# Performance work log

Hardware: AMD Instinct MI355X
Metric: run time of the kernel (lower is better)

## Reference

```python
import jax, jax.numpy as jnp
import numpy as np

NUM_STATES = 64
HIDDEN = 32
NUM_ACTIONS = 3
SEQ_LEN = 512
BATCH = 2048


def setup_inputs() -> dict:
    key = jax.random.key(0)
    ks = jax.random.split(key, 7)
    s_ih = 1.0 / np.sqrt(HIDDEN)
    x = jax.random.normal(ks[0], (SEQ_LEN, BATCH, NUM_STATES), dtype=jnp.float32)
    # PyTorch LSTM params: gate order [i, f, g, o], each block of size HIDDEN
    W_ih = jax.random.uniform(ks[1], (4 * HIDDEN, NUM_STATES), minval=-s_ih, maxval=s_ih, dtype=jnp.float32)
    W_hh = jax.random.uniform(ks[2], (4 * HIDDEN, HIDDEN), minval=-s_ih, maxval=s_ih, dtype=jnp.float32)
    b_ih = jax.random.uniform(ks[3], (4 * HIDDEN,), minval=-s_ih, maxval=s_ih, dtype=jnp.float32)
    b_hh = jax.random.uniform(ks[4], (4 * HIDDEN,), minval=-s_ih, maxval=s_ih, dtype=jnp.float32)
    s_d = 1.0 / np.sqrt(HIDDEN)
    W_d = jax.random.uniform(ks[5], (NUM_ACTIONS, HIDDEN), minval=-s_d, maxval=s_d, dtype=jnp.float32)
    b_d = jax.random.uniform(ks[6], (NUM_ACTIONS,), minval=-s_d, maxval=s_d, dtype=jnp.float32)
    return {"x": x, "W_ih": W_ih, "W_hh": W_hh, "b_ih": b_ih, "b_hh": b_hh, "W_d": W_d, "b_d": b_d}


def _lstm_last_hidden(x, W_ih, W_hh, b_ih, b_hh):
    # x: [T, B, F] time-major, as in nn.LSTM(batch_first=False)
    B = x.shape[1]
    H = W_hh.shape[1]
    # Precompute input projections for all timesteps in one GEMM: [T, B, 4H]
    x_proj = jnp.einsum('tbf,gf->tbg', x, W_ih) + (b_ih + b_hh)

    def step(carry, xp_t):
        h, c = carry
        gates = xp_t + h @ W_hh.T  # [B, 4H]
        i, f, g, o = jnp.split(gates, 4, axis=-1)
        i = jax.nn.sigmoid(i)
        f = jax.nn.sigmoid(f)
        g = jnp.tanh(g)
        o = jax.nn.sigmoid(o)
        c = f * c + i * g
        h = o * jnp.tanh(c)
        return (h, c), None

    h0 = jnp.zeros((B, H), dtype=x.dtype)
    c0 = jnp.zeros((B, H), dtype=x.dtype)
    (h_T, _), _ = jax.lax.scan(step, (h0, c0), x_proj)
    return h_T  # [B, H] == lstm output at last timestep (x[-1,:,:])


def reference(x, W_ih, W_hh, b_ih, b_hh, W_d, b_d):
    h_T = _lstm_last_hidden(x, W_ih, W_hh, b_ih, b_hh)
    h = jax.nn.relu(h_T)
    return h @ W_d.T + b_d  # [B, num_actions]
```

## Files before the change

kernel.cpp:

```cpp
#include <hip/hip_runtime.h>

typedef __bf16 bf16_t;
typedef __bf16 bf16x8 __attribute__((ext_vector_type(8)));
typedef float  f32x4  __attribute__((ext_vector_type(4)));
typedef unsigned int u32x4 __attribute__((ext_vector_type(4)));

#define T_STEPS 512
#define BATCH   2048
#define NS      64
#define FSTR    36

#define K_SIG  (-1.4426950408889634f)
#define K_TANH ( 2.8853900817779268f)

#define MFMA(A, B, C) __builtin_amdgcn_mfma_f32_16x16x32_bf16((A), (B), (C), 0, 0, 0)
#define RCPE(xv) __builtin_amdgcn_rcpf(1.0f + __builtin_amdgcn_exp2f(xv))

__device__ __forceinline__ void barrier_lgkm() {
  asm volatile("s_waitcnt lgkmcnt(0)\n\ts_barrier" ::: "memory");
}

__global__ __launch_bounds__(256, 1) __attribute__((amdgpu_waves_per_eu(1, 1)))
void lstm_policy_kernel(const float* __restrict__ x,
                        const float* __restrict__ W_ih,
                        const float* __restrict__ W_hh,
                        const float* __restrict__ b_ih,
                        const float* __restrict__ b_hh,
                        const float* __restrict__ W_d,
                        const float* __restrict__ b_d,
                        float* __restrict__ out)
{
  __shared__ unsigned int hlds[2][4][64];
  __shared__ float hf[16 * FSTR];

  const int tid  = threadIdx.x;
  const int wv   = tid >> 6;
  const int lane = tid & 63;
  const int m    = lane & 15;
  const int q    = lane >> 4;
  const int U    = wv >> 1;
  const int rsel = wv & 1;
  const int row0 = blockIdx.x << 4;

  bf16x8 a_ih[4][2], a_hh[4];
  f32x4  bias[4];
  #pragma unroll
  for (int G = 0; G < 4; ++G) {
    const float k = (G == 2) ? K_TANH : K_SIG;
    const int wrow = (G << 5) + (U << 4) + m;
    const float* pih = W_ih + wrow * 64;
    const float* phh = W_hh + (wrow << 5);
    #pragma unroll
    for (int j = 0; j < 8; ++j) {
      a_ih[G][0][j] = (bf16_t)(k * pih[(q << 3) + j]);
      a_ih[G][1][j] = (bf16_t)(k * pih[32 + (q << 3) + j]);
      const int us = (j < 4) ? ((q << 2) + j) : (16 + (q << 2) + (j - 4));
      a_hh[G][j] = (bf16_t)(k * phh[us]);
    }
    #pragma unroll
    for (int r = 0; r < 4; ++r) {
      const int u = (G << 5) + (U << 4) + (q << 2) + r;
      bias[G][r] = (b_ih[u] + b_hh[u]) * k;
    }
  }

  const size_t xstep = (size_t)BATCH * NS;
  const float* xb = x + (size_t)row0 * NS;
  const int    lo = m * NS + (q << 3);

  f32x4 xf[4][4];
  {
    const float* p1 = xb + 1 * xstep + lo;
    const float* p2 = xb + 2 * xstep + lo;
    const float* p3 = xb + 3 * xstep + lo;
    const float* p4 = xb + 4 * xstep + lo;
    xf[1][0]=*(const f32x4*)(p1); xf[1][1]=*(const f32x4*)(p1+4); xf[1][2]=*(const f32x4*)(p1+32); xf[1][3]=*(const f32x4*)(p1+36);
    xf[2][0]=*(const f32x4*)(p2); xf[2][1]=*(const f32x4*)(p2+4); xf[2][2]=*(const f32x4*)(p2+32); xf[2][3]=*(const f32x4*)(p2+36);
    xf[3][0]=*(const f32x4*)(p3); xf[3][1]=*(const f32x4*)(p3+4); xf[3][2]=*(const f32x4*)(p3+32); xf[3][3]=*(const f32x4*)(p3+36);
    xf[0][0]=*(const f32x4*)(p4); xf[0][1]=*(const f32x4*)(p4+4); xf[0][2]=*(const f32x4*)(p4+32); xf[0][3]=*(const f32x4*)(p4+36);
  }

  f32x4 acc[4];
  {
    const float* p0 = xb + lo;
    f32x4 x0a = *(const f32x4*)(p0),      x0b = *(const f32x4*)(p0 + 4);
    f32x4 x0c = *(const f32x4*)(p0 + 32), x0d = *(const f32x4*)(p0 + 36);
    bf16x8 xA, xB;
    #pragma unroll
    for (int j = 0; j < 4; ++j) {
      xA[j] = (bf16_t)x0a[j]; xA[4+j] = (bf16_t)x0b[j];
      xB[j] = (bf16_t)x0c[j]; xB[4+j] = (bf16_t)x0d[j];
    }
    #pragma unroll
    for (int G = 0; G < 4; ++G) {
      acc[G] = MFMA(a_ih[G][0], xA, bias[G]);
      acc[G] = MFMA(a_ih[G][1], xB, acc[G]);
    }
  }

  float cst[2] = {0.0f, 0.0f};
  bf16x8 hB = {};

  #define CELL(RR, E, HOUT)                                                         \
    {                                                                               \
      const float iv = RCPE(gr[0][RR]);                                             \
      const float fv = RCPE(gr[1][RR]);                                             \
      const float rg = RCPE(gr[2][RR]);                                             \
      const float ov = RCPE(gr[3][RR]);                                             \
      const float gs = __builtin_fmaf(-2.0f * K_TANH, rg, K_TANH);   \
      const float cn = __builtin_fmaf(fv, cst[E], iv * gs);           \
      cst[E] = cn;                                                                  \
      const float rh  = RCPE(cn);                                                   \
      const float ov2 = ov + ov;                                                    \
      HOUT = __builtin_fmaf(-ov2, rh, ov);                           \
      if (tt == T_STEPS - 1) hf[m * FSTR + (U << 4) + (q << 2) + RR] = fmaxf(HOUT, 0.0f); \
    }

  #define STEP(P)                                                                   \
  do {                                                                              \
    const int tt  = t + (P);                                                        \
    const int par = (P) & 1;                                                        \
    f32x4 gr[4];                                                                    \
    _Pragma("unroll")                                                               \
    for (int G = 0; G < 4; ++G)                                                     \
      gr[G] = MFMA(a_hh[G], hB, acc[G]);                                            \
    float h0, h1;                                                                   \
    if (rsel == 0) { CELL(0, 0, h0) CELL(1, 1, h1) }                                \
    else           { CELL(2, 0, h0) CELL(3, 1, h1) }                                \
    {                                                                               \
      const unsigned int s0 = __builtin_bit_cast(unsigned short, (bf16_t)h0);       \
      const unsigned int s1 = __builtin_bit_cast(unsigned short, (bf16_t)h1);       \
      hlds[par][wv][lane] = s0 | (s1 << 16);                                        \
    }                                                                               \
    barrier_lgkm();                                                                 \
    const unsigned int w0 = hlds[par][0][lane];                                     \
    const unsigned int w1 = hlds[par][1][lane];                                     \
    const unsigned int w2 = hlds[par][2][lane];                                     \
    const unsigned int w3 = hlds[par][3][lane];                                     \
                \
    {                                                                               \
      const int ns = ((P) + 1) & 3;                                                 \
      bf16x8 xA, xB;                                                                \
      _Pragma("unroll")                                                             \
      for (int j = 0; j < 4; ++j) {                                                 \
        xA[j] = (bf16_t)xf[ns][0][j]; xA[4+j] = (bf16_t)xf[ns][1][j];               \
        xB[j] = (bf16_t)xf[ns][2][j]; xB[4+j] = (bf16_t)xf[ns][3][j];               \
      }                                                                             \
      _Pragma("unroll")                                                             \
      for (int G = 0; G < 4; ++G) {                                                 \
        acc[G] = MFMA(a_ih[G][0], xA, bias[G]);                                     \
        acc[G] = MFMA(a_ih[G][1], xB, acc[G]);                                      \
      }                                                                             \
      int tp = tt + 5; if (tp > T_STEPS - 1) tp = T_STEPS - 1;                      \
      const float* pf = xb + (size_t)tp * xstep + lo;                               \
      xf[ns][0] = *(const f32x4*)(pf);                                              \
      xf[ns][1] = *(const f32x4*)(pf + 4);                                          \
      xf[ns][2] = *(const f32x4*)(pf + 32);                                         \
      xf[ns][3] = *(const f32x4*)(pf + 36);                                         \
    }                                                                               \
    {                                                                               \
      u32x4 hw; hw[0] = w0; hw[1] = w1; hw[2] = w2; hw[3] = w3;                     \
      hB = __builtin_bit_cast(bf16x8, hw);                                          \
    }                                                                               \
  } while (0)

  #pragma unroll 1
  for (int t = 0; t < T_STEPS; t += 4) {
    STEP(0);
    STEP(1);
    STEP(2);
    STEP(3);
  }
  #undef STEP
  #undef CELL

  __syncthreads();

  if (tid < 48) {
    const int r = tid / 3;
    const int a = tid - r * 3;
    float s = b_d[a];
    #pragma unroll
    for (int u = 0; u < 32; ++u)
      s += hf[r * FSTR + u] * W_d[a * 32 + u];
    out[(size_t)(row0 + r) * 3 + a] = s;
  }
}

extern "C" void kernel_launch(void* const* d_in, const int* in_sizes, int n_in,
                              void* d_out, int out_size, void* d_ws, size_t ws_size,
                              hipStream_t stream) {
  const float* x    = (const float*)d_in[0];
  const float* W_ih = (const float*)d_in[1];
  const float* W_hh = (const float*)d_in[2];
  const float* b_ih = (const float*)d_in[3];
  const float* b_hh = (const float*)d_in[4];
  const float* W_d  = (const float*)d_in[5];
  const float* b_d  = (const float*)d_in[6];
  float* out = (float*)d_out;

  dim3 grid(BATCH / 16);
  dim3 block(256);
  hipLaunchKernelGGL(lstm_policy_kernel, grid, block, 0, stream,
                     x, W_ih, W_hh, b_ih, b_hh, W_d, b_d, out);
}
```

Before: 526.6 us.

## Stream x tiles into LDS via async global_load_lds ring buffer

Replaces the per-thread register prefetch of x (a 4-deep f32x4 ring) with direct global-to-LDS async loads into an 8-slot swizzled LDS ring, issued DPF=6 steps ahead. Each step now reads its x tile from LDS with XOR-swizzled offsets before the recurrent MFMAs, and waits on vmcnt before the barrier. It also drops the waves_per_eu attribute. The aim is to free registers and hide global latency better, at the cost of more LDS traffic and a vmcnt wait on the serial critical path.

```diff
diff --git a/kernel.cpp b/kernel.cpp
--- a/kernel.cpp
+++ b/kernel.cpp
@@ -9,6 +9,8 @@
 #define BATCH   2048
 #define NS      64
 #define FSTR    36
+#define NSLOT   8
+#define DPF     6
 
 #define K_SIG  (-1.4426950408889634f)
 #define K_TANH ( 2.8853900817779268f)
@@ -20,7 +22,13 @@
   asm volatile("s_waitcnt lgkmcnt(0)\n\ts_barrier" ::: "memory");
 }
 
-__global__ __launch_bounds__(256, 1) __attribute__((amdgpu_waves_per_eu(1, 1)))
+__device__ __forceinline__ void async_load16(const float* g, char* l) {
+  __builtin_amdgcn_global_load_lds(
+      (const __attribute__((address_space(1))) void*)g,
+      (__attribute__((address_space(3))) void*)l, 16, 0, 0);
+}
+
+__global__ __launch_bounds__(256, 1)
 void lstm_policy_kernel(const float* __restrict__ x,
                         const float* __restrict__ W_ih,
                         const float* __restrict__ W_hh,
@@ -30,6 +38,7 @@
                         const float* __restrict__ b_d,
                         float* __restrict__ out)
 {
+  __shared__ char  xlds[NSLOT * 4096];
   __shared__ unsigned int hlds[2][4][64];
   __shared__ float hf[16 * FSTR];
 
@@ -66,30 +75,37 @@
 
   const size_t xstep = (size_t)BATCH * NS;
   const float* xb = x + (size_t)row0 * NS;
-  const int    lo = m * NS + (q << 3);
-
-  f32x4 xf[4][4];
-  {
-    const float* p1 = xb + 1 * xstep + lo;
-    const float* p2 = xb + 2 * xstep + lo;
-    const float* p3 = xb + 3 * xstep + lo;
-    const float* p4 = xb + 4 * xstep + lo;
-    xf[1][0]=*(const f32x4*)(p1); xf[1][1]=*(const f32x4*)(p1+4); xf[1][2]=*(const f32x4*)(p1+32); xf[1][3]=*(const f32x4*)(p1+36);
-    xf[2][0]=*(const f32x4*)(p2); xf[2][1]=*(const f32x4*)(p2+4); xf[2][2]=*(const f32x4*)(p2+32); xf[2][3]=*(const f32x4*)(p2+36);
-    xf[3][0]=*(const f32x4*)(p3); xf[3][1]=*(const f32x4*)(p3+4); xf[3][2]=*(const f32x4*)(p3+32); xf[3][3]=*(const f32x4*)(p3+36);
-    xf[0][0]=*(const f32x4*)(p4); xf[0][1]=*(const f32x4*)(p4+4); xf[0][2]=*(const f32x4*)(p4+32); xf[0][3]=*(const f32x4*)(p4+36);
-  }
+
+  const int slin = (wv << 10) + (lane << 4);
+  const int ssrc = slin ^ (((slin >> 8) & 7) << 4);
+  const float* gsrc = xb + (ssrc >> 2);
+  char* const lqbase = xlds + (wv << 10);
+
+  const int rb  = m * 256 + (q << 5);
+  const int sw  = (m & 7) << 4;
+  const int ro0 = rb ^ sw;
+  const int ro1 = (rb + 16) ^ sw;
+  const int ro2 = (rb + 128) ^ sw;
+  const int ro3 = (rb + 144) ^ sw;
+
+  #pragma unroll
+  for (int s = 0; s < DPF; ++s)
+    async_load16(gsrc + (size_t)s * xstep, lqbase + (s << 12));
+  asm volatile("s_waitcnt vmcnt(4)" ::: "memory");
+  __syncthreads();
 
   f32x4 acc[4];
   {
-    const float* p0 = xb + lo;
-    f32x4 x0a = *(const f32x4*)(p0),      x0b = *(const f32x4*)(p0 + 4);
-    f32x4 x0c = *(const f32x4*)(p0 + 32), x0d = *(const f32x4*)(p0 + 36);
+    const char* sp = xlds;
+    const f32x4 xr0 = *(const f32x4*)(sp + ro0);
+    const f32x4 xr1 = *(const f32x4*)(sp + ro1);
+    const f32x4 xr2 = *(const f32x4*)(sp + ro2);
+    const f32x4 xr3 = *(const f32x4*)(sp + ro3);
     bf16x8 xA, xB;
     #pragma unroll
     for (int j = 0; j < 4; ++j) {
-      xA[j] = (bf16_t)x0a[j]; xA[4+j] = (bf16_t)x0b[j];
-      xB[j] = (bf16_t)x0c[j]; xB[4+j] = (bf16_t)x0d[j];
+      xA[j] = (bf16_t)xr0[j]; xA[4+j] = (bf16_t)xr1[j];
+      xB[j] = (bf16_t)xr2[j]; xB[4+j] = (bf16_t)xr3[j];
     }
     #pragma unroll
     for (int G = 0; G < 4; ++G) {
@@ -120,10 +136,18 @@
   do {                                                                              \
     const int tt  = t + (P);                                                        \
     const int par = (P) & 1;                                                        \
+                \
+    const char* sp = xlds + (((tt + 1) & 7) << 12);                                 \
+    const f32x4 xr0 = *(const f32x4*)(sp + ro0);                                    \
+    const f32x4 xr1 = *(const f32x4*)(sp + ro1);                                    \
+    const f32x4 xr2 = *(const f32x4*)(sp + ro2);                                    \
+    const f32x4 xr3 = *(const f32x4*)(sp + ro3);                                    \
+                                                               \
     f32x4 gr[4];                                                                    \
     _Pragma("unroll")                                                               \
     for (int G = 0; G < 4; ++G)                                                     \
       gr[G] = MFMA(a_hh[G], hB, acc[G]);                                            \
+                                   \
     float h0, h1;                                                                   \
     if (rsel == 0) { CELL(0, 0, h0) CELL(1, 1, h1) }                                \
     else           { CELL(2, 0, h0) CELL(3, 1, h1) }                                \
@@ -132,32 +156,34 @@
       const unsigned int s1 = __builtin_bit_cast(unsigned short, (bf16_t)h1);       \
       hlds[par][wv][lane] = s0 | (s1 << 16);                                        \
     }                                                                               \
+          \
+    {                                                                               \
+      int tp = tt + DPF; if (tp > T_STEPS - 1) tp = T_STEPS - 1;                    \
+      async_load16(gsrc + (size_t)tp * xstep, lqbase + ((tp & 7) << 12));           \
+    }                                                                               \
+                                            \
+    asm volatile("s_waitcnt vmcnt(4)" ::: "memory");                                \
     barrier_lgkm();                                                                 \
+                                     \
     const unsigned int w0 = hlds[par][0][lane];                                     \
     const unsigned int w1 = hlds[par][1][lane];                                     \
     const unsigned int w2 = hlds[par][2][lane];                                     \
     const unsigned int w3 = hlds[par][3][lane];                                     \
-                \
-    {                                                                               \
-      const int ns = ((P) + 1) & 3;                                                 \
+                                        \
+    {                                                                               \
       bf16x8 xA, xB;                                                                \
       _Pragma("unroll")                                                             \
       for (int j = 0; j < 4; ++j) {                                                 \
-        xA[j] = (bf16_t)xf[ns][0][j]; xA[4+j] = (bf16_t)xf[ns][1][j];               \
-        xB[j] = (bf16_t)xf[ns][2][j]; xB[4+j] = (bf16_t)xf[ns][3][j];               \
+        xA[j] = (bf16_t)xr0[j]; xA[4+j] = (bf16_t)xr1[j];                           \
+        xB[j] = (bf16_t)xr2[j]; xB[4+j] = (bf16_t)xr3[j];                           \
       }                                                                             \
       _Pragma("unroll")                                                             \
       for (int G = 0; G < 4; ++G) {                                                 \
         acc[G] = MFMA(a_ih[G][0], xA, bias[G]);                                     \
         acc[G] = MFMA(a_ih[G][1], xB, acc[G]);                                      \
       }                                                                             \
-      int tp = tt + 5; if (tp > T_STEPS - 1) tp = T_STEPS - 1;                      \
-      const float* pf = xb + (size_t)tp * xstep + lo;                               \
-      xf[ns][0] = *(const f32x4*)(pf);                                              \
-      xf[ns][1] = *(const f32x4*)(pf + 4);                                          \
-      xf[ns][2] = *(const f32x4*)(pf + 32);                                         \
-      xf[ns][3] = *(const f32x4*)(pf + 36);                                         \
-    }                                                                               \
+    }                                                                               \
+                                                           \
     {                                                                               \
       u32x4 hw; hw[0] = w0; hw[1] = w1; hw[2] = w2; hw[3] = w3;                     \
       hB = __builtin_bit_cast(bf16x8, hw);                                          \
```

Result: slower. 629.2 us (+19.5%).

## Split LSTM cell work across eight waves and pair sigmoids under one reciprocal

Applied to the files above, without the earlier changes.

The block grows from 256 to 512 threads, so each wave handles one accumulator row of the gate tile instead of two. Each wave writes its bf16 hidden value to LDS as a 16-bit store instead of a packed 32-bit word. Sigmoid pairs (i,f) and (g,o) now share one reciprocal through the identity 1/((1+a)(1+b)), which cuts transcendental ops on the serial recurrence path. The trade-off is that every wave redundantly issues the same MFMAs and x loads, there are more waves at the barrier, and the launch bounds change to allow two blocks per CU.

```diff
diff --git a/kernel.cpp b/kernel.cpp
--- a/kernel.cpp
+++ b/kernel.cpp
@@ -14,13 +14,12 @@
 #define K_TANH ( 2.8853900817779268f)
 
 #define MFMA(A, B, C) __builtin_amdgcn_mfma_f32_16x16x32_bf16((A), (B), (C), 0, 0, 0)
-#define RCPE(xv) __builtin_amdgcn_rcpf(1.0f + __builtin_amdgcn_exp2f(xv))
 
 __device__ __forceinline__ void barrier_lgkm() {
   asm volatile("s_waitcnt lgkmcnt(0)\n\ts_barrier" ::: "memory");
 }
 
-__global__ __launch_bounds__(256, 1) __attribute__((amdgpu_waves_per_eu(1, 1)))
+__global__ __launch_bounds__(512, 2)
 void lstm_policy_kernel(const float* __restrict__ x,
                         const float* __restrict__ W_ih,
                         const float* __restrict__ W_hh,
@@ -38,8 +37,8 @@
   const int lane = tid & 63;
   const int m    = lane & 15;
   const int q    = lane >> 4;
-  const int U    = wv >> 1;
-  const int rsel = wv & 1;
+  const int U    = wv >> 2;
+  const int r3   = wv & 3;
   const int row0 = blockIdx.x << 4;
 
   bf16x8 a_ih[4][2], a_hh[4];
@@ -98,22 +97,34 @@
     }
   }
 
-  float cst[2] = {0.0f, 0.0f};
-  bf16x8 hB = {};
-
-  #define CELL(RR, E, HOUT)                                                         \
+  float  cst = 0.0f;
+  bf16x8 hB  = {};
+
+  #define CELLX(RR)                                                                 \
     {                                                                               \
-      const float iv = RCPE(gr[0][RR]);                                             \
-      const float fv = RCPE(gr[1][RR]);                                             \
-      const float rg = RCPE(gr[2][RR]);                                             \
-      const float ov = RCPE(gr[3][RR]);                                             \
+      const float Ai = __builtin_amdgcn_exp2f(gr[0][RR]);                           \
+      const float Af = __builtin_amdgcn_exp2f(gr[1][RR]);                           \
+      const float Ag = __builtin_amdgcn_exp2f(gr[2][RR]);                           \
+      const float Ao = __builtin_amdgcn_exp2f(gr[3][RR]);                           \
+      const float rif = __builtin_amdgcn_rcpf(                                      \
+          __builtin_fmaf(Ai, Af, Ai + Af) + 1.0f);                                  \
+      const float iv = __builtin_fmaf(Af, rif, rif);                  \
+      const float fv = __builtin_fmaf(Ai, rif, rif);                  \
+      const float rgo = __builtin_amdgcn_rcpf(                                      \
+          __builtin_fmaf(Ag, Ao, Ag + Ao) + 1.0f);                                  \
+      const float rg = __builtin_fmaf(Ao, rgo, rgo);                  \
+      const float ov = __builtin_fmaf(Ag, rgo, rgo);                  \
       const float gs = __builtin_fmaf(-2.0f * K_TANH, rg, K_TANH);   \
-      const float cn = __builtin_fmaf(fv, cst[E], iv * gs);           \
-      cst[E] = cn;                                                                  \
-      const float rh  = RCPE(cn);                                                   \
+      const float cn = __builtin_fmaf(fv, cst, iv * gs);              \
+      cst = cn;                                                                     \
+      const float rh  = __builtin_amdgcn_rcpf(1.0f + __builtin_amdgcn_exp2f(cn));   \
       const float ov2 = ov + ov;                                                    \
-      HOUT = __builtin_fmaf(-ov2, rh, ov);                           \
-      if (tt == T_STEPS - 1) hf[m * FSTR + (U << 4) + (q << 2) + RR] = fmaxf(HOUT, 0.0f); \
+      const float h   = __builtin_fmaf(-ov2, rh, ov);                \
+      const unsigned short hs =                                                     \
+          __builtin_bit_cast(unsigned short, (bf16_t)h);                            \
+      ((unsigned short*)&hlds[par][(U << 1) | ((RR) >> 1)][lane])[(RR) & 1] = hs;   \
+      if (tt == T_STEPS - 1)                                                        \
+        hf[m * FSTR + (U << 4) + (q << 2) + (RR)] = fmaxf(h, 0.0f);                 \
     }
 
   #define STEP(P)                                                                   \
@@ -124,20 +135,16 @@
     _Pragma("unroll")                                                               \
     for (int G = 0; G < 4; ++G)                                                     \
       gr[G] = MFMA(a_hh[G], hB, acc[G]);                                            \
-    float h0, h1;                                                                   \
-    if (rsel == 0) { CELL(0, 0, h0) CELL(1, 1, h1) }                                \
-    else           { CELL(2, 0, h0) CELL(3, 1, h1) }                                \
-    {                                                                               \
-      const unsigned int s0 = __builtin_bit_cast(unsigned short, (bf16_t)h0);       \
-      const unsigned int s1 = __builtin_bit_cast(unsigned short, (bf16_t)h1);       \
-      hlds[par][wv][lane] = s0 | (s1 << 16);                                        \
-    }                                                                               \
+    if      (r3 == 0) CELLX(0)                                                      \
+    else if (r3 == 1) CELLX(1)                                                      \
+    else if (r3 == 2) CELLX(2)                                                      \
+    else              CELLX(3)                                                      \
     barrier_lgkm();                                                                 \
     const unsigned int w0 = hlds[par][0][lane];                                     \
     const unsigned int w1 = hlds[par][1][lane];                                     \
     const unsigned int w2 = hlds[par][2][lane];                                     \
     const unsigned int w3 = hlds[par][3][lane];                                     \
-                \
+                    \
     {                                                                               \
       const int ns = ((P) + 1) & 3;                                                 \
       bf16x8 xA, xB;                                                                \
@@ -172,7 +179,7 @@
     STEP(3);
   }
   #undef STEP
-  #undef CELL
+  #undef CELLX
 
   __syncthreads();
 
@@ -200,7 +207,7 @@
   float* out = (float*)d_out;
 
   dim3 grid(BATCH / 16);
-  dim3 block(256);
+  dim3 block(512);
   hipLaunchKernelGGL(lstm_policy_kernel, grid, block, 0, stream,
                      x, W_ih, W_hh, b_ih, b_hh, W_d, b_d, out);
 }
```

After: 723.0 us. 37.3% more time.
